# Optimization experiments

Measured on AMD Instinct MI355X. Metric: run time of the kernel, lower is better.

The kernel has to match this reference:

```python
import jax, jax.numpy as jnp
import numpy as np

HIDDEN = 1024
N_EMB = 4096
K_TOP = 64
EPS = 1e-6


def rmsnorm(x, w):
    xf = x.astype(jnp.float32)
    y = xf * jax.lax.rsqrt(jnp.mean(xf * xf, axis=-1, keepdims=True) + EPS)
    return y.astype(x.dtype) * w


def setup_inputs() -> dict:
    key = jax.random.key(0)
    ks = jax.random.split(key, 5)
    B, S, D, N = 16, 2048, HIDDEN, N_EMB
    bound = 1.0 / np.sqrt(D)  # torch Linear reset_parameters uniform bound
    return {
        "X": jax.random.normal(ks[0], (B, S, D), dtype=jnp.float32),
        "alpha": jnp.zeros((), dtype=jnp.float32),
        "E": jax.random.normal(ks[1], (N, D), dtype=jnp.float32) / np.sqrt(D),
        "Wq": jax.random.uniform(ks[2], (D, D), dtype=jnp.float32, minval=-bound, maxval=bound),
        "Wk": jax.random.uniform(ks[3], (D, D), dtype=jnp.float32, minval=-bound, maxval=bound),
        "xn_w": jnp.ones((D,), dtype=jnp.float32),
        "sn_w": jnp.ones((D,), dtype=jnp.float32),
        "on_w": jnp.ones((D,), dtype=jnp.float32),
    }


def reference(X, alpha, E, Wq, Wk, xn_w, sn_w, on_w):
    scale = HIDDEN ** (-0.5)
    Xn = rmsnorm(X, xn_w)            # (B,S,D)
    En = rmsnorm(E, sn_w)            # (N,D)
    Q = Xn @ Wq.T                    # (B,S,D)
    Km = En @ Wk.T                   # (N,D)
    scores = jnp.einsum('bsd,nd->bsn', Q, Km) * scale  # (B,S,N)
    global_scores = jnp.max(scores, axis=1)            # (B,N)
    top_vals, _ = jax.lax.top_k(global_scores, K_TOP)
    cutoff = top_vals[:, -1:]                          # (B,1)
    masked = jnp.where(global_scores >= cutoff, global_scores, -jnp.inf)
    dense_w = jax.nn.softmax(global_scores, axis=-1)
    sparse_w = jax.nn.softmax(masked, axis=-1)
    weights = alpha * dense_w + (1.0 - alpha) * sparse_w  # (B,N)
    O = rmsnorm(weights @ En, on_w)                      # (B,D)
    return O, weights
```

## Files before the change

### kernel.cpp

```cpp
#include <hip/hip_runtime.h>


namespace {

constexpr int D_DIM = 1024;
constexpr int NE    = 4096;
constexpr int BATCH = 16;
constexpr int SEQ   = 2048;
constexpr int MX    = BATCH * SEQ;
constexpr int KTOP  = 64;
constexpr int CAND  = 128;
constexpr int BK    = 32;

using f32x4  = __attribute__((ext_vector_type(4))) float;
using bf16x8 = __attribute__((ext_vector_type(8))) short;
using i32x4  = __attribute__((ext_vector_type(4))) int;

__device__ inline unsigned encf(float f) {
  unsigned u = __float_as_uint(f);
  return (u & 0x80000000u) ? ~u : (u | 0x80000000u);
}
__device__ inline float decf(unsigned e) {
  unsigned u = (e & 0x80000000u) ? (e ^ 0x80000000u) : ~e;
  return __uint_as_float(u);
}

__device__ inline unsigned short f2bf(float f) {
  unsigned u = __float_as_uint(f);
  unsigned lsb = (u >> 16) & 1u;
  u += 0x7fffu + lsb;
  return (unsigned short)(u >> 16);
}
__device__ inline float bf2f(unsigned short h) {
  return __uint_as_float(((unsigned)h) << 16);
}

__device__ inline void gload16(const void* gsrc, void* ldst) {
  __builtin_amdgcn_global_load_lds(
      (const __attribute__((address_space(1))) unsigned int*)gsrc,
      (__attribute__((address_space(3))) unsigned int*)ldst, 16, 0, 0);
}

#define LGK0_SB() do { asm volatile("s_waitcnt lgkmcnt(0)" ::: "memory"); \
                       __builtin_amdgcn_sched_barrier(0); } while (0)

__global__ void row_rinv_k(const float* __restrict__ X, float* __restrict__ rinv) {
  __shared__ float l4[4];
  int row = blockIdx.x;
  float4 v = ((const float4*)(X + (size_t)row * D_DIM))[threadIdx.x];
  float ss = v.x * v.x + v.y * v.y + v.z * v.z + v.w * v.w;
  for (int o = 32; o > 0; o >>= 1) ss += __shfl_xor(ss, o);
  int lane = threadIdx.x & 63, w = threadIdx.x >> 6;
  if (lane == 0) l4[w] = ss;
  __syncthreads();
  if (threadIdx.x == 0) {
    float t = l4[0] + l4[1] + l4[2] + l4[3];
    rinv[row] = rsqrtf(t * (1.0f / D_DIM) + 1e-6f);
  }
}

__global__ void rinv_quantx_k(const float* __restrict__ X, float* __restrict__ rinv,
                              float* __restrict__ sxr, int* __restrict__ XQ) {
  __shared__ float l4[4], m4[4];
  int row = blockIdx.x;
  float4 v = ((const float4*)(X + (size_t)row * D_DIM))[threadIdx.x];
  float ss = v.x * v.x + v.y * v.y + v.z * v.z + v.w * v.w;
  float am = fmaxf(fmaxf(fabsf(v.x), fabsf(v.y)), fmaxf(fabsf(v.z), fabsf(v.w)));
  for (int o = 32; o > 0; o >>= 1) {
    ss += __shfl_xor(ss, o);
    am = fmaxf(am, __shfl_xor(am, o));
  }
  int lane = threadIdx.x & 63, w = threadIdx.x >> 6;
  if (lane == 0) { l4[w] = ss; m4[w] = am; }
  __syncthreads();
  float t  = l4[0] + l4[1] + l4[2] + l4[3];
  float amax = fmaxf(fmaxf(m4[0], m4[1]), fmaxf(m4[2], m4[3]));
  amax = fmaxf(amax, 1e-30f);
  float ri = rsqrtf(t * (1.0f / D_DIM) + 1e-6f);
  if (threadIdx.x == 0) {
    rinv[row] = ri;
    sxr[row]  = ri * amax * (1.0f / 127.0f);
  }
  float qs = 127.0f / amax;
  int q0 = (int)rintf(v.x * qs) & 0xff;
  int q1 = (int)rintf(v.y * qs) & 0xff;
  int q2 = (int)rintf(v.z * qs) & 0xff;
  int q3 = (int)rintf(v.w * qs) & 0xff;
  XQ[(size_t)row * 256 + threadIdx.x] = q0 | (q1 << 8) | (q2 << 16) | (q3 << 24);
}

__global__ void quant_p_k(const unsigned short* __restrict__ PH,
                          const unsigned short* __restrict__ PL,
                          float* __restrict__ sp, int* __restrict__ PQ) {
  __shared__ float m4[4];
  int row = blockIdx.x;
  ushort4 h = *(const ushort4*)(PH + (size_t)row * D_DIM + threadIdx.x * 4);
  ushort4 l = *(const ushort4*)(PL + (size_t)row * D_DIM + threadIdx.x * 4);
  float p0 = bf2f(h.x) + bf2f(l.x);
  float p1 = bf2f(h.y) + bf2f(l.y);
  float p2 = bf2f(h.z) + bf2f(l.z);
  float p3 = bf2f(h.w) + bf2f(l.w);
  float am = fmaxf(fmaxf(fabsf(p0), fabsf(p1)), fmaxf(fabsf(p2), fabsf(p3)));
  for (int o = 32; o > 0; o >>= 1) am = fmaxf(am, __shfl_xor(am, o));
  int lane = threadIdx.x & 63, w = threadIdx.x >> 6;
  if (lane == 0) m4[w] = am;
  __syncthreads();
  float amax = fmaxf(fmaxf(m4[0], m4[1]), fmaxf(m4[2], m4[3]));
  amax = fmaxf(amax, 1e-30f);
  if (threadIdx.x == 0) sp[row] = amax * (1.0f / 127.0f);
  float qs = 127.0f / amax;
  int q0 = (int)rintf(p0 * qs) & 0xff;
  int q1 = (int)rintf(p1 * qs) & 0xff;
  int q2 = (int)rintf(p2 * qs) & 0xff;
  int q3 = (int)rintf(p3 * qs) & 0xff;
  PQ[(size_t)row * 256 + threadIdx.x] = q0 | (q1 << 8) | (q2 << 16) | (q3 << 24);
}

__global__ void split_wt_k(const float* __restrict__ W, const float* __restrict__ cw,
                           unsigned short* __restrict__ H, unsigned short* __restrict__ L) {
  __shared__ float t[32][33];
  int k0 = blockIdx.x * 32, d0 = blockIdx.y * 32;
  int tx = threadIdx.x & 31, ty4 = (threadIdx.x >> 5) * 4;
#pragma unroll
  for (int i = 0; i < 4; ++i)
    t[ty4 + i][tx] = W[(size_t)(d0 + ty4 + i) * D_DIM + k0 + tx];
  __syncthreads();
#pragma unroll
  for (int i = 0; i < 4; ++i) {
    int a = ty4 + i;
    float v = t[tx][a] * cw[k0 + a];
    unsigned short h = f2bf(v);
    H[(size_t)(k0 + a) * D_DIM + d0 + tx] = h;
    L[(size_t)(k0 + a) * D_DIM + d0 + tx] = f2bf(v - bf2f(h));
  }
}

__global__ void transpose_k(const float* __restrict__ W, float* __restrict__ T) {
  __shared__ float t[32][33];
  int x0 = blockIdx.x * 32, y0 = blockIdx.y * 32;
  int tx = threadIdx.x & 31, ty4 = (threadIdx.x >> 5) * 4;
#pragma unroll
  for (int i = 0; i < 4; ++i)
    t[ty4 + i][tx] = W[(size_t)(y0 + ty4 + i) * D_DIM + x0 + tx];
  __syncthreads();
#pragma unroll
  for (int i = 0; i < 4; ++i)
    T[(size_t)(x0 + ty4 + i) * D_DIM + y0 + tx] = t[tx][ty4 + i];
}

template <int FPOUT>
__global__ __launch_bounds__(256, 2) void gemm_a32_k(
    const float* __restrict__ A, const float* __restrict__ rinv,
    const unsigned short* __restrict__ BH, const unsigned short* __restrict__ BL,
    unsigned short* __restrict__ OH, unsigned short* __restrict__ OL,
    float* __restrict__ Of) {
  __shared__ __align__(16) float lA[128 * 32];
  __shared__ __align__(16) unsigned short lBH[128 * 32];
  __shared__ __align__(16) unsigned short lBL[128 * 32];
  __shared__ float ldsR[128];

  int tid = threadIdx.x;
  int lane = tid & 63, wid = tid >> 6;
  int wr = wid >> 1, wc = wid & 1;
  int fr = lane & 15, fg = lane >> 4;
  long m0 = (long)blockIdx.x * 128;
  long n0 = (long)blockIdx.y * 128;

  if (tid < 128) ldsR[tid] = rinv ? rinv[m0 + tid] : 1.0f;

  f32x4 acc[4][4] = {};

  for (int kk = 0; kk < D_DIM; kk += BK) {
#pragma unroll
    for (int i = 0; i < 4; ++i) {
      int chunk = i * 256 + tid;
      int r = chunk >> 3, c = chunk & 7;
      int cs = c ^ (r & 7);
      const float* src = A + (m0 + r) * (long)D_DIM + kk + cs * 4;
      gload16(src, (void*)(lA + ((i * 256 + (tid & ~63)) << 2)));
    }
#pragma unroll
    for (int i = 0; i < 2; ++i) {
      int chunk = i * 256 + tid;
      int r = chunk >> 2, c = chunk & 3;
      int cs = c ^ ((r >> 1) & 3);
      long boff = (n0 + r) * (long)D_DIM + kk + cs * 8;
      int lo = (i * 256 + (tid & ~63)) << 3;
      gload16(BH + boff, (void*)(lBH + lo));
      gload16(BL + boff, (void*)(lBL + lo));
    }
    __syncthreads();

    bf16x8 aH[4], aL[4], bH[4], bL[4];
#pragma unroll
    for (int m = 0; m < 4; ++m) {
      int row = wr * 64 + m * 16 + fr;
      int rm = row & 7;
      f32x4 p0 = *(const f32x4*)(lA + row * 32 + (((fg * 2 + 0) ^ rm) * 4));
      f32x4 p1 = *(const f32x4*)(lA + row * 32 + (((fg * 2 + 1) ^ rm) * 4));
#pragma unroll
      for (int e = 0; e < 8; ++e) {
        float f = (e < 4) ? p0[e] : p1[e - 4];
        unsigned short h = f2bf(f);
        aH[m][e] = (short)h;
        aL[m][e] = (short)f2bf(f - bf2f(h));
      }
    }
#pragma unroll
    for (int n = 0; n < 4; ++n) {
      int row = wc * 64 + n * 16 + fr;
      int sc = fg ^ ((row >> 1) & 3);
      bH[n] = *(const bf16x8*)(lBH + row * 32 + sc * 8);
      bL[n] = *(const bf16x8*)(lBL + row * 32 + sc * 8);
    }
#pragma unroll
    for (int m = 0; m < 4; ++m)
#pragma unroll
      for (int n = 0; n < 4; ++n) {
        acc[m][n] = __builtin_amdgcn_mfma_f32_16x16x32_bf16(aH[m], bH[n], acc[m][n], 0, 0, 0);
        acc[m][n] = __builtin_amdgcn_mfma_f32_16x16x32_bf16(aH[m], bL[n], acc[m][n], 0, 0, 0);
        acc[m][n] = __builtin_amdgcn_mfma_f32_16x16x32_bf16(aL[m], bH[n], acc[m][n], 0, 0, 0);
      }
    __syncthreads();
  }

#pragma unroll
  for (int m = 0; m < 4; ++m) {
#pragma unroll
    for (int j = 0; j < 4; ++j) {
      int rloc = wr * 64 + m * 16 + fg * 4 + j;
      float rv = ldsR[rloc];
      long grow = m0 + rloc;
#pragma unroll
      for (int n = 0; n < 4; ++n) {
        long gcol = n0 + wc * 64 + n * 16 + fr;
        float v = acc[m][n][j] * rv;
        if (FPOUT) {
          Of[grow * D_DIM + gcol] = v;
        } else {
          unsigned short h = f2bf(v);
          OH[grow * D_DIM + gcol] = h;
          OL[grow * D_DIM + gcol] = f2bf(v - bf2f(h));
        }
      }
    }
  }
}

__global__ __launch_bounds__(512, 2) void gemm_scores1_k(
    const signed char* __restrict__ XQ, const signed char* __restrict__ PQ,
    const float* __restrict__ sxr, const float* __restrict__ sp,
    unsigned* __restrict__ gmax) {
  __shared__ __align__(16) signed char lA[2][256 * 64];
  __shared__ __align__(16) signed char lB[2][256 * 64];
  __shared__ float ldsR[256];

  int tid = threadIdx.x;
  int lane = tid & 63, wid = tid >> 6;
  int wr = wid >> 2;
  int wcn = wid & 3;
  int fr = lane & 15, fg = lane >> 4;

  int id = blockIdx.x;
  int xcd = id & 7;
  int r = id >> 3;
  int tile_m = xcd * 16 + (r >> 4);
  int tile_n = r & 15;
  long m0 = (long)tile_m * 256;
  long n0 = (long)tile_n * 256;

  if (tid < 256) ldsR[tid] = sxr[m0 + tid];

  auto stageTile = [&](int buf, int kt) {
    int kk = kt * 64;
#pragma unroll
    for (int i = 0; i < 2; ++i) {
      int chunk = i * 512 + tid;
      int r2 = chunk >> 2, c = chunk & 3;
      int cs = c ^ ((r2 >> 1) & 3);
      gload16(XQ + (m0 + r2) * (long)D_DIM + kk + cs * 16,
              (void*)(&lA[buf][0] + ((i * 512 + (tid & ~63)) << 4)));
    }
#pragma unroll
    for (int i = 0; i < 2; ++i) {
      int chunk = i * 512 + tid;
      int r2 = chunk >> 2, c = chunk & 3;
      int cs = c ^ ((r2 >> 1) & 3);
      gload16(PQ + (n0 + r2) * (long)D_DIM + kk + cs * 16,
              (void*)(&lB[buf][0] + ((i * 512 + (tid & ~63)) << 4)));
    }
  };

  i32x4 acc[8][4] = {};

  stageTile(0, 0);
  stageTile(1, 1);
  asm volatile("s_waitcnt lgkmcnt(0)" ::: "memory");

  i32x4 aF[4], bF[4];

  for (int kt = 0; kt < 16; ++kt) {
    int cur = kt & 1;
    const signed char* As = &lA[cur][0];
    const signed char* Bs = &lB[cur][0];

    if (kt < 15) {
      asm volatile("s_waitcnt vmcnt(4)" ::: "memory");
    } else {
      asm volatile("s_waitcnt vmcnt(0)" ::: "memory");
    }
    __builtin_amdgcn_s_barrier();

#pragma unroll
    for (int mi = 0; mi < 4; ++mi) {
      int row = wr * 128 + mi * 16 + fr;
      int ck = fg ^ ((row >> 1) & 3);
      aF[mi] = *(const i32x4*)(As + row * 64 + ck * 16);
    }
#pragma unroll
    for (int ni = 0; ni < 2; ++ni) {
      int row = wcn * 64 + ni * 16 + fr;
      int ck = fg ^ ((row >> 1) & 3);
      bF[ni] = *(const i32x4*)(Bs + row * 64 + ck * 16);
    }
    LGK0_SB();
    __builtin_amdgcn_s_setprio(1);
#pragma unroll
    for (int mi = 0; mi < 4; ++mi)
#pragma unroll
      for (int ni = 0; ni < 2; ++ni)
        acc[mi][ni] = __builtin_amdgcn_mfma_i32_16x16x64_i8(
            aF[mi], bF[ni], acc[mi][ni], 0, 0, 0);
    __builtin_amdgcn_s_setprio(0);

#pragma unroll
    for (int ni = 2; ni < 4; ++ni) {
      int row = wcn * 64 + ni * 16 + fr;
      int ck = fg ^ ((row >> 1) & 3);
      bF[ni] = *(const i32x4*)(Bs + row * 64 + ck * 16);
    }
    LGK0_SB();
    __builtin_amdgcn_s_setprio(1);
#pragma unroll
    for (int mi = 0; mi < 4; ++mi)
#pragma unroll
      for (int ni = 2; ni < 4; ++ni)
        acc[mi][ni] = __builtin_amdgcn_mfma_i32_16x16x64_i8(
            aF[mi], bF[ni], acc[mi][ni], 0, 0, 0);
    __builtin_amdgcn_s_setprio(0);

#pragma unroll
    for (int mi = 0; mi < 4; ++mi) {
      int row = wr * 128 + (mi + 4) * 16 + fr;
      int ck = fg ^ ((row >> 1) & 3);
      aF[mi] = *(const i32x4*)(As + row * 64 + ck * 16);
    }
    LGK0_SB();
    __builtin_amdgcn_s_barrier();
    if (kt + 2 < 16) stageTile(cur, kt + 2);
    __builtin_amdgcn_s_setprio(1);
#pragma unroll
    for (int mi = 0; mi < 4; ++mi)
#pragma unroll
      for (int ni = 2; ni < 4; ++ni)
        acc[mi + 4][ni] = __builtin_amdgcn_mfma_i32_16x16x64_i8(
            aF[mi], bF[ni], acc[mi + 4][ni], 0, 0, 0);
    __builtin_amdgcn_s_setprio(0);

    __builtin_amdgcn_s_setprio(1);
#pragma unroll
    for (int mi = 0; mi < 4; ++mi)
#pragma unroll
      for (int ni = 0; ni < 2; ++ni)
        acc[mi + 4][ni] = __builtin_amdgcn_mfma_i32_16x16x64_i8(
            aF[mi], bF[ni], acc[mi + 4][ni], 0, 0, 0);
    __builtin_amdgcn_s_setprio(0);
  }

  int b = (int)(m0 >> 11);
#pragma unroll
  for (int ni = 0; ni < 4; ++ni) {
    long col = n0 + wcn * 64 + ni * 16 + fr;
    float spc = sp[col];
    float v = -3.0e38f;
#pragma unroll
    for (int mi = 0; mi < 8; ++mi)
#pragma unroll
      for (int j = 0; j < 4; ++j) {
        int row = wr * 128 + mi * 16 + fg * 4 + j;
        v = fmaxf(v, (float)acc[mi][ni][j] * ldsR[row]);
      }
    v *= spc;
    v = fmaxf(v, __shfl_xor(v, 16));
    v = fmaxf(v, __shfl_xor(v, 32));
    if (fg == 0) {
      atomicMax(&gmax[(long)b * NE + col], encf(v * 0.03125f));
    }
  }
}

__global__ void cand_select_k(const unsigned* __restrict__ gmax,
                              int* __restrict__ candIdx, unsigned* __restrict__ gmax2) {
  __shared__ unsigned enc[NE];
  __shared__ int ic[257];
  int tid = threadIdx.x;
  int lane = tid & 63, w = tid >> 6;
  int zb = blockIdx.x;
  if (tid < CAND) gmax2[zb * CAND + tid] = 0u;
  const unsigned* g = gmax + (size_t)zb * NE;
  for (int i = tid; i < NE; i += 256) enc[i] = g[i];
  __syncthreads();

  unsigned cur = 0;
  for (int bit = 31; bit >= 0; --bit) {
    unsigned cand = cur | (1u << bit);
    int c = 0;
    for (int i = tid; i < NE; i += 256) c += (enc[i] >= cand) ? 1 : 0;
    for (int o = 32; o > 0; o >>= 1) c += __shfl_xor(c, o);
    __syncthreads();
    if (lane == 0) ic[w] = c;
    __syncthreads();
    int tot = ic[0] + ic[1] + ic[2] + ic[3];
    if (tot >= CAND) cur = cand;
  }

  int myc = 0;
  for (int i = tid; i < NE; i += 256) myc += (enc[i] >= cur) ? 1 : 0;
  __syncthreads();
  ic[tid] = myc;
  __syncthreads();
  if (tid == 0) {
    int s = 0;
    for (int t = 0; t < 256; ++t) { int v = ic[t]; ic[t] = s; s += v; }
  }
  __syncthreads();
  int off = ic[tid];
  for (int i = tid; i < NE; i += 256)
    if (enc[i] >= cur) {
      if (off < CAND) candIdx[zb * CAND + off] = i;
      ++off;
    }
}

__global__ void gather_k(const unsigned short* __restrict__ PH,
                         const unsigned short* __restrict__ PL,
                         const int* __restrict__ candIdx,
                         unsigned short* __restrict__ cPH,
                         unsigned short* __restrict__ cPL) {
  int j = blockIdx.x;
  int zb = blockIdx.y;
  int n = candIdx[zb * CAND + j];
  int t4 = threadIdx.x * 4;
  size_t dst = ((size_t)(zb * CAND + j)) * D_DIM + t4;
  size_t src = (size_t)n * D_DIM + t4;
  *(ushort4*)(cPH + dst) = *(const ushort4*)(PH + src);
  *(ushort4*)(cPL + dst) = *(const ushort4*)(PL + src);
}

__global__ __launch_bounds__(256, 2) void gemm_rescore_k(
    const float* __restrict__ X, const float* __restrict__ rinvA,
    const unsigned short* __restrict__ cPH, const unsigned short* __restrict__ cPL,
    unsigned* __restrict__ gmax2) {
  __shared__ __align__(16) float lA[128 * 32];
  __shared__ __align__(16) unsigned short lBH[128 * 32], lBL[128 * 32];
  __shared__ float ldsR[128];

  int tid = threadIdx.x;
  int lane = tid & 63, wid = tid >> 6;
  int wr = wid >> 1, wc = wid & 1;
  int fr = lane & 15, fg = lane >> 4;
  int z = blockIdx.z;
  long m0 = (long)blockIdx.x * 128;
  long arow0 = (long)z * SEQ + m0;
  long brow0 = (long)z * CAND;

  if (tid < 128) ldsR[tid] = rinvA[arow0 + tid];

  f32x4 acc[4][4] = {};

  for (int kk = 0; kk < D_DIM; kk += BK) {
#pragma unroll
    for (int i = 0; i < 4; ++i) {
      int chunk = i * 256 + tid;
      int r = chunk >> 3, c = chunk & 7;
      int cs = c ^ (r & 7);
      const float* src = X + (arow0 + r) * (long)D_DIM + kk + cs * 4;
      gload16(src, (void*)(lA + ((i * 256 + (tid & ~63)) << 2)));
    }
#pragma unroll
    for (int i = 0; i < 2; ++i) {
      int chunk = i * 256 + tid;
      int r = chunk >> 2, c = chunk & 3;
      int cs = c ^ ((r >> 1) & 3);
      long boff = (brow0 + r) * (long)D_DIM + kk + cs * 8;
      int lo = (i * 256 + (tid & ~63)) << 3;
      gload16(cPH + boff, (void*)(lBH + lo));
      gload16(cPL + boff, (void*)(lBL + lo));
    }
    __syncthreads();

    bf16x8 aH[4], aL[4], bH[4], bL[4];
#pragma unroll
    for (int m = 0; m < 4; ++m) {
      int row = wr * 64 + m * 16 + fr;
      int rm = row & 7;
      f32x4 p0 = *(const f32x4*)(lA + row * 32 + (((fg * 2 + 0) ^ rm) * 4));
      f32x4 p1 = *(const f32x4*)(lA + row * 32 + (((fg * 2 + 1) ^ rm) * 4));
#pragma unroll
      for (int e = 0; e < 8; ++e) {
        float f = (e < 4) ? p0[e] : p1[e - 4];
        unsigned short h = f2bf(f);
        aH[m][e] = (short)h;
        aL[m][e] = (short)f2bf(f - bf2f(h));
      }
    }
#pragma unroll
    for (int n = 0; n < 4; ++n) {
      int row = wc * 64 + n * 16 + fr;
      int sc = fg ^ ((row >> 1) & 3);
      bH[n] = *(const bf16x8*)(lBH + row * 32 + sc * 8);
      bL[n] = *(const bf16x8*)(lBL + row * 32 + sc * 8);
    }
#pragma unroll
    for (int m = 0; m < 4; ++m)
#pragma unroll
      for (int n = 0; n < 4; ++n) {
        acc[m][n] = __builtin_amdgcn_mfma_f32_16x16x32_bf16(aH[m], bH[n], acc[m][n], 0, 0, 0);
        acc[m][n] = __builtin_amdgcn_mfma_f32_16x16x32_bf16(aH[m], bL[n], acc[m][n], 0, 0, 0);
        acc[m][n] = __builtin_amdgcn_mfma_f32_16x16x32_bf16(aL[m], bH[n], acc[m][n], 0, 0, 0);
      }
    __syncthreads();
  }

#pragma unroll
  for (int n = 0; n < 4; ++n) {
    float v = -3.0e38f;
#pragma unroll
    for (int m = 0; m < 4; ++m)
#pragma unroll
      for (int j = 0; j < 4; ++j) {
        float rv = ldsR[wr * 64 + m * 16 + fg * 4 + j];
        v = fmaxf(v, acc[m][n][j] * rv);
      }
    v = fmaxf(v, __shfl_xor(v, 16));
    v = fmaxf(v, __shfl_xor(v, 32));
    if (fg == 0) {
      int col = wc * 64 + n * 16 + fr;
      atomicMax(&gmax2[z * CAND + col], encf(v * 0.03125f));
    }
  }
}

__global__ void scatter_k(const unsigned* __restrict__ gmax2,
                          const int* __restrict__ candIdx,
                          unsigned* __restrict__ gmax) {
  int z = blockIdx.x, j = threadIdx.x;
  int n = candIdx[z * CAND + j];
  gmax[(size_t)z * NE + n] = gmax2[z * CAND + j];
}

__global__ void topk_weights_k(const unsigned* __restrict__ gmax,
                               const float* __restrict__ alpha_p,
                               float* __restrict__ wout, int* __restrict__ idx,
                               int* __restrict__ cnt) {
  __shared__ unsigned enc[NE];
  __shared__ unsigned ubc[4];
  __shared__ float l4[4];
  __shared__ int ic[257];
  int tid = threadIdx.x;
  int lane = tid & 63, w = tid >> 6;
  const unsigned* g = gmax + (size_t)blockIdx.x * NE;
  for (int i = tid; i < NE; i += 256) enc[i] = g[i];
  __syncthreads();

  unsigned mx = 0;
  for (int i = tid; i < NE; i += 256) mx = enc[i] > mx ? enc[i] : mx;
  for (int o = 32; o > 0; o >>= 1) {
    unsigned other = (unsigned)__shfl_xor((int)mx, o);
    if (other > mx) mx = other;
  }
  if (lane == 0) ubc[w] = mx;
  __syncthreads();
  unsigned m1e = ubc[0];
  for (int t = 1; t < 4; ++t) m1e = ubc[t] > m1e ? ubc[t] : m1e;
  float m1 = decf(m1e);

  unsigned cur = 0;
  for (int bit = 31; bit >= 0; --bit) {
    unsigned cand = cur | (1u << bit);
    int c = 0;
    for (int i = tid; i < NE; i += 256) c += (enc[i] >= cand) ? 1 : 0;
    for (int o = 32; o > 0; o >>= 1) c += __shfl_xor(c, o);
    __syncthreads();
    if (lane == 0) ic[w] = c;
    __syncthreads();
    int tot = ic[0] + ic[1] + ic[2] + ic[3];
    if (tot >= KTOP) cur = cand;
  }

  float sd = 0.f, ssum = 0.f;
  for (int i = tid; i < NE; i += 256) {
    float e = expf(decf(enc[i]) - m1);
    sd += e;
    if (enc[i] >= cur) ssum += e;
  }
  for (int o = 32; o > 0; o >>= 1) { sd += __shfl_xor(sd, o); ssum += __shfl_xor(ssum, o); }
  __syncthreads();
  if (lane == 0) { l4[w] = sd; }
  __syncthreads();
  float SD = l4[0] + l4[1] + l4[2] + l4[3];
  __syncthreads();
  if (lane == 0) { l4[w] = ssum; }
  __syncthreads();
  float SS = l4[0] + l4[1] + l4[2] + l4[3];

  float alpha = alpha_p[0];
  float wd = alpha / SD;
  float ws_ = (1.0f - alpha) / SS;
  for (int i = tid; i < NE; i += 256) {
    float e = expf(decf(enc[i]) - m1);
    float wv = wd * e + ((enc[i] >= cur) ? ws_ * e : 0.0f);
    wout[(size_t)blockIdx.x * NE + i] = wv;
  }

  int myc = 0;
  for (int i = tid; i < NE; i += 256) myc += (enc[i] >= cur) ? 1 : 0;
  __syncthreads();
  ic[tid] = myc;
  __syncthreads();
  if (tid == 0) {
    int s = 0;
    for (int t = 0; t < 256; ++t) { int v = ic[t]; ic[t] = s; s += v; }
    ic[256] = s;
    cnt[blockIdx.x] = s;
  }
  __syncthreads();
  int off = ic[tid];
  for (int i = tid; i < NE; i += 256)
    if (enc[i] >= cur) idx[(size_t)blockIdx.x * NE + (off++)] = i;
}

__global__ void out_o_k(const float* __restrict__ wts, const float* __restrict__ E,
                        const float* __restrict__ rinvE, const float* __restrict__ sn_w,
                        const float* __restrict__ on_w, const float* __restrict__ alpha_p,
                        const int* __restrict__ idx, const int* __restrict__ cnt,
                        float* __restrict__ O) {
  __shared__ float l4[4];
  int b = blockIdx.x, tid = threadIdx.x;
  float acc[4] = {0.f, 0.f, 0.f, 0.f};
  float alpha = alpha_p[0];
  if (alpha == 0.0f) {
    int nsel = cnt[b];
    for (int j = 0; j < nsel; ++j) {
      int n = idx[(size_t)b * NE + j];
      float wv = wts[(size_t)b * NE + n] * rinvE[n];
      const float* er = E + (size_t)n * D_DIM;
#pragma unroll
      for (int i = 0; i < 4; ++i) acc[i] += wv * er[tid + 256 * i];
    }
  } else {
    for (int n = 0; n < NE; ++n) {
      float wv = wts[(size_t)b * NE + n] * rinvE[n];
      const float* er = E + (size_t)n * D_DIM;
#pragma unroll
      for (int i = 0; i < 4; ++i) acc[i] += wv * er[tid + 256 * i];
    }
  }
  float ssq = 0.f;
#pragma unroll
  for (int i = 0; i < 4; ++i) {
    acc[i] *= sn_w[tid + 256 * i];
    ssq += acc[i] * acc[i];
  }
  for (int o = 32; o > 0; o >>= 1) ssq += __shfl_xor(ssq, o);
  int lane = tid & 63, w = tid >> 6;
  if (lane == 0) l4[w] = ssq;
  __syncthreads();
  float tot = l4[0] + l4[1] + l4[2] + l4[3];
  float r = rsqrtf(tot * (1.0f / D_DIM) + 1e-6f);
#pragma unroll
  for (int i = 0; i < 4; ++i)
    O[(size_t)b * D_DIM + tid + 256 * i] = acc[i] * r * on_w[tid + 256 * i];
}

}

extern "C" void kernel_launch(void* const* d_in, const int* in_sizes, int n_in,
                              void* d_out, int out_size, void* d_ws, size_t ws_size,
                              hipStream_t stream) {
  const float* X     = (const float*)d_in[0];
  const float* alpha = (const float*)d_in[1];
  const float* E     = (const float*)d_in[2];
  const float* Wq    = (const float*)d_in[3];
  const float* Wk    = (const float*)d_in[4];
  const float* xn_w  = (const float*)d_in[5];
  const float* sn_w  = (const float*)d_in[6];
  const float* on_w  = (const float*)d_in[7];
  float* O    = (float*)d_out;
  float* Wout = (float*)d_out + (size_t)BATCH * D_DIM;

  char* ws = (char*)d_ws;
  size_t off = 0;
  auto alloc = [&](size_t bytes) {
    char* p = ws + off;
    off += (bytes + 255) & ~(size_t)255;
    return p;
  };
  signed char*    XQ    = (signed char*)alloc((size_t)MX * D_DIM);
  signed char*    PQ    = (signed char*)alloc((size_t)NE * D_DIM);
  float*          WqTf  = (float*)alloc((size_t)D_DIM * D_DIM * 4);
  unsigned short* WkTH  = (unsigned short*)alloc((size_t)D_DIM * D_DIM * 2);
  unsigned short* WkTL  = (unsigned short*)alloc((size_t)D_DIM * D_DIM * 2);
  unsigned short* W2TH  = (unsigned short*)alloc((size_t)D_DIM * D_DIM * 2);
  unsigned short* W2TL  = (unsigned short*)alloc((size_t)D_DIM * D_DIM * 2);
  unsigned short* PH    = (unsigned short*)alloc((size_t)NE * D_DIM * 2);
  unsigned short* PL    = (unsigned short*)alloc((size_t)NE * D_DIM * 2);
  unsigned short* cPH   = (unsigned short*)alloc((size_t)BATCH * CAND * D_DIM * 2);
  unsigned short* cPL   = (unsigned short*)alloc((size_t)BATCH * CAND * D_DIM * 2);
  float* rinvX = (float*)alloc((size_t)MX * 4);
  float* sxr   = (float*)alloc((size_t)MX * 4);
  float* rinvE = (float*)alloc((size_t)NE * 4);
  float* sp    = (float*)alloc((size_t)NE * 4);
  unsigned* gmax  = (unsigned*)alloc((size_t)BATCH * NE * 4);
  unsigned* gmax2 = (unsigned*)alloc((size_t)BATCH * CAND * 4);
  int* candIdx = (int*)alloc((size_t)BATCH * CAND * 4);
  int* idx = (int*)alloc((size_t)BATCH * NE * 4);
  int* cnt = (int*)alloc((size_t)BATCH * 4);
  if (off > ws_size) return;

  hipMemsetAsync(gmax, 0, (size_t)BATCH * NE * 4, stream);

  row_rinv_k<<<NE, 256, 0, stream>>>(E, rinvE);
  transpose_k<<<dim3(D_DIM / 32, D_DIM / 32), 256, 0, stream>>>(Wq, WqTf);
  split_wt_k<<<dim3(D_DIM / 32, D_DIM / 32), 256, 0, stream>>>(Wk, sn_w, WkTH, WkTL);
  gemm_a32_k<0><<<dim3(8, 8), 256, 0, stream>>>(
      WqTf, xn_w, WkTH, WkTL, W2TH, W2TL, nullptr);
  gemm_a32_k<0><<<dim3(NE / 128, D_DIM / 128), 256, 0, stream>>>(
      E, rinvE, W2TH, W2TL, PH, PL, nullptr);
  quant_p_k<<<NE, 256, 0, stream>>>(PH, PL, sp, (int*)PQ);

  rinv_quantx_k<<<MX, 256, 0, stream>>>(X, rinvX, sxr, (int*)XQ);
  gemm_scores1_k<<<(MX / 256) * (NE / 256), 512, 0, stream>>>(XQ, PQ, sxr, sp, gmax);

  cand_select_k<<<BATCH, 256, 0, stream>>>(gmax, candIdx, gmax2);
  gather_k<<<dim3(CAND, BATCH), 256, 0, stream>>>(PH, PL, candIdx, cPH, cPL);
  gemm_rescore_k<<<dim3(SEQ / 128, 1, BATCH), 256, 0, stream>>>(
      X, rinvX, cPH, cPL, gmax2);
  scatter_k<<<BATCH, CAND, 0, stream>>>(gmax2, candIdx, gmax);

  topk_weights_k<<<BATCH, 256, 0, stream>>>(gmax, alpha, Wout, idx, cnt);
  out_o_k<<<BATCH, 256, 0, stream>>>(Wout, E, rinvE, sn_w, on_w, alpha, idx, cnt, O);
}
```

Measured before the change: 438.3 us.

## Fuse small kernels, gather candidate rows in-GEMM, and reorder score tile schedule

Merges the Wq transpose and Wk split into one prep kernel, and drops the separate gather kernel so the rescore GEMM reads candidate rows of PH/PL directly through candIdx. It merges scatter, top-k weights and output accumulation into one final kernel that keeps the selection in shared memory. It also changes the block-to-tile mapping in the int8 scores GEMM to alter cache locality. Together these cut launch count and intermediate global traffic, at the cost of more shared memory in the final kernel and non-contiguous B loads in the rescore GEMM.

New measurement: 415.9 us. -5.1%, faster.

```diff
diff --git a/kernel.cpp b/kernel.cpp
--- a/kernel.cpp
+++ b/kernel.cpp
@@ -116,36 +116,27 @@
   PQ[(size_t)row * 256 + threadIdx.x] = q0 | (q1 << 8) | (q2 << 16) | (q3 << 24);
 }
 
-__global__ void split_wt_k(const float* __restrict__ W, const float* __restrict__ cw,
-                           unsigned short* __restrict__ H, unsigned short* __restrict__ L) {
-  __shared__ float t[32][33];
+__global__ void prep_w_k(const float* __restrict__ Wq, const float* __restrict__ Wk,
+                         const float* __restrict__ cw, float* __restrict__ T,
+                         unsigned short* __restrict__ H, unsigned short* __restrict__ L) {
+  __shared__ float t[32][33], u[32][33];
   int k0 = blockIdx.x * 32, d0 = blockIdx.y * 32;
   int tx = threadIdx.x & 31, ty4 = (threadIdx.x >> 5) * 4;
 #pragma unroll
-  for (int i = 0; i < 4; ++i)
-    t[ty4 + i][tx] = W[(size_t)(d0 + ty4 + i) * D_DIM + k0 + tx];
+  for (int i = 0; i < 4; ++i) {
+    t[ty4 + i][tx] = Wq[(size_t)(d0 + ty4 + i) * D_DIM + k0 + tx];
+    u[ty4 + i][tx] = Wk[(size_t)(d0 + ty4 + i) * D_DIM + k0 + tx];
+  }
   __syncthreads();
 #pragma unroll
   for (int i = 0; i < 4; ++i) {
     int a = ty4 + i;
-    float v = t[tx][a] * cw[k0 + a];
+    T[(size_t)(k0 + a) * D_DIM + d0 + tx] = t[tx][a];
+    float v = u[tx][a] * cw[k0 + a];
     unsigned short h = f2bf(v);
     H[(size_t)(k0 + a) * D_DIM + d0 + tx] = h;
     L[(size_t)(k0 + a) * D_DIM + d0 + tx] = f2bf(v - bf2f(h));
   }
-}
-
-__global__ void transpose_k(const float* __restrict__ W, float* __restrict__ T) {
-  __shared__ float t[32][33];
-  int x0 = blockIdx.x * 32, y0 = blockIdx.y * 32;
-  int tx = threadIdx.x & 31, ty4 = (threadIdx.x >> 5) * 4;
-#pragma unroll
-  for (int i = 0; i < 4; ++i)
-    t[ty4 + i][tx] = W[(size_t)(y0 + ty4 + i) * D_DIM + x0 + tx];
-  __syncthreads();
-#pragma unroll
-  for (int i = 0; i < 4; ++i)
-    T[(size_t)(x0 + ty4 + i) * D_DIM + y0 + tx] = t[tx][ty4 + i];
 }
 
 template <int FPOUT>
@@ -264,8 +255,8 @@
   int id = blockIdx.x;
   int xcd = id & 7;
   int r = id >> 3;
-  int tile_m = xcd * 16 + (r >> 4);
-  int tile_n = r & 15;
+  int tile_n = (r & 7) | ((r >> 7) << 3);
+  int tile_m = xcd * 16 + ((r >> 3) & 15);
   long m0 = (long)tile_m * 256;
   long n0 = (long)tile_n * 256;
 
@@ -442,25 +433,10 @@
     }
 }
 
-__global__ void gather_k(const unsigned short* __restrict__ PH,
-                         const unsigned short* __restrict__ PL,
-                         const int* __restrict__ candIdx,
-                         unsigned short* __restrict__ cPH,
-                         unsigned short* __restrict__ cPL) {
-  int j = blockIdx.x;
-  int zb = blockIdx.y;
-  int n = candIdx[zb * CAND + j];
-  int t4 = threadIdx.x * 4;
-  size_t dst = ((size_t)(zb * CAND + j)) * D_DIM + t4;
-  size_t src = (size_t)n * D_DIM + t4;
-  *(ushort4*)(cPH + dst) = *(const ushort4*)(PH + src);
-  *(ushort4*)(cPL + dst) = *(const ushort4*)(PL + src);
-}
-
 __global__ __launch_bounds__(256, 2) void gemm_rescore_k(
     const float* __restrict__ X, const float* __restrict__ rinvA,
-    const unsigned short* __restrict__ cPH, const unsigned short* __restrict__ cPL,
-    unsigned* __restrict__ gmax2) {
+    const unsigned short* __restrict__ PH, const unsigned short* __restrict__ PL,
+    const int* __restrict__ candIdx, unsigned* __restrict__ gmax2) {
   __shared__ __align__(16) float lA[128 * 32];
   __shared__ __align__(16) unsigned short lBH[128 * 32], lBL[128 * 32];
   __shared__ float ldsR[128];
@@ -472,9 +448,15 @@
   int z = blockIdx.z;
   long m0 = (long)blockIdx.x * 128;
   long arow0 = (long)z * SEQ + m0;
-  long brow0 = (long)z * CAND;
 
   if (tid < 128) ldsR[tid] = rinvA[arow0 + tid];
+
+  long bbase[2];
+#pragma unroll
+  for (int i = 0; i < 2; ++i) {
+    int r = (i * 256 + tid) >> 2;
+    bbase[i] = (long)candIdx[z * CAND + r] * D_DIM;
+  }
 
   f32x4 acc[4][4] = {};
 
@@ -492,10 +474,10 @@
       int chunk = i * 256 + tid;
       int r = chunk >> 2, c = chunk & 3;
       int cs = c ^ ((r >> 1) & 3);
-      long boff = (brow0 + r) * (long)D_DIM + kk + cs * 8;
+      long boff = bbase[i] + kk + cs * 8;
       int lo = (i * 256 + (tid & ~63)) << 3;
-      gload16(cPH + boff, (void*)(lBH + lo));
-      gload16(cPL + boff, (void*)(lBL + lo));
+      gload16(PH + boff, (void*)(lBH + lo));
+      gload16(PL + boff, (void*)(lBL + lo));
     }
     __syncthreads();
 
@@ -551,26 +533,25 @@
   }
 }
 
-__global__ void scatter_k(const unsigned* __restrict__ gmax2,
-                          const int* __restrict__ candIdx,
-                          unsigned* __restrict__ gmax) {
-  int z = blockIdx.x, j = threadIdx.x;
-  int n = candIdx[z * CAND + j];
-  gmax[(size_t)z * NE + n] = gmax2[z * CAND + j];
-}
-
-__global__ void topk_weights_k(const unsigned* __restrict__ gmax,
-                               const float* __restrict__ alpha_p,
-                               float* __restrict__ wout, int* __restrict__ idx,
-                               int* __restrict__ cnt) {
+__global__ void final_k(const unsigned* __restrict__ gmax,
+                        const unsigned* __restrict__ gmax2,
+                        const int* __restrict__ candIdx,
+                        const float* __restrict__ alpha_p,
+                        const float* __restrict__ E, const float* __restrict__ rinvE,
+                        const float* __restrict__ sn_w, const float* __restrict__ on_w,
+                        float* __restrict__ wout, float* __restrict__ O) {
   __shared__ unsigned enc[NE];
+  __shared__ int sel[NE];
   __shared__ unsigned ubc[4];
   __shared__ float l4[4];
   __shared__ int ic[257];
   int tid = threadIdx.x;
   int lane = tid & 63, w = tid >> 6;
-  const unsigned* g = gmax + (size_t)blockIdx.x * NE;
+  int b = blockIdx.x;
+  const unsigned* g = gmax + (size_t)b * NE;
   for (int i = tid; i < NE; i += 256) enc[i] = g[i];
+  __syncthreads();
+  if (tid < CAND) enc[candIdx[b * CAND + tid]] = gmax2[b * CAND + tid];
   __syncthreads();
 
   unsigned mx = 0;
@@ -620,7 +601,7 @@
   for (int i = tid; i < NE; i += 256) {
     float e = expf(decf(enc[i]) - m1);
     float wv = wd * e + ((enc[i] >= cur) ? ws_ * e : 0.0f);
-    wout[(size_t)blockIdx.x * NE + i] = wv;
+    wout[(size_t)b * NE + i] = wv;
   }
 
   int myc = 0;
@@ -632,35 +613,29 @@
     int s = 0;
     for (int t = 0; t < 256; ++t) { int v = ic[t]; ic[t] = s; s += v; }
     ic[256] = s;
-    cnt[blockIdx.x] = s;
   }
   __syncthreads();
   int off = ic[tid];
   for (int i = tid; i < NE; i += 256)
-    if (enc[i] >= cur) idx[(size_t)blockIdx.x * NE + (off++)] = i;
-}
-
-__global__ void out_o_k(const float* __restrict__ wts, const float* __restrict__ E,
-                        const float* __restrict__ rinvE, const float* __restrict__ sn_w,
-                        const float* __restrict__ on_w, const float* __restrict__ alpha_p,
-                        const int* __restrict__ idx, const int* __restrict__ cnt,
-                        float* __restrict__ O) {
-  __shared__ float l4[4];
-  int b = blockIdx.x, tid = threadIdx.x;
+    if (enc[i] >= cur) sel[off++] = i;
+  __syncthreads();
+  int nsel = ic[256];
+
   float acc[4] = {0.f, 0.f, 0.f, 0.f};
-  float alpha = alpha_p[0];
   if (alpha == 0.0f) {
-    int nsel = cnt[b];
+    float coef = wd + ws_;
     for (int j = 0; j < nsel; ++j) {
-      int n = idx[(size_t)b * NE + j];
-      float wv = wts[(size_t)b * NE + n] * rinvE[n];
+      int n = sel[j];
+      float e = expf(decf(enc[n]) - m1);
+      float wv = coef * e * rinvE[n];
       const float* er = E + (size_t)n * D_DIM;
 #pragma unroll
       for (int i = 0; i < 4; ++i) acc[i] += wv * er[tid + 256 * i];
     }
   } else {
     for (int n = 0; n < NE; ++n) {
-      float wv = wts[(size_t)b * NE + n] * rinvE[n];
+      float e = expf(decf(enc[n]) - m1);
+      float wv = (wd * e + ((enc[n] >= cur) ? ws_ * e : 0.0f)) * rinvE[n];
       const float* er = E + (size_t)n * D_DIM;
 #pragma unroll
       for (int i = 0; i < 4; ++i) acc[i] += wv * er[tid + 256 * i];
@@ -673,14 +648,13 @@
     ssq += acc[i] * acc[i];
   }
   for (int o = 32; o > 0; o >>= 1) ssq += __shfl_xor(ssq, o);
-  int lane = tid & 63, w = tid >> 6;
   if (lane == 0) l4[w] = ssq;
   __syncthreads();
   float tot = l4[0] + l4[1] + l4[2] + l4[3];
-  float r = rsqrtf(tot * (1.0f / D_DIM) + 1e-6f);
+  float rn = rsqrtf(tot * (1.0f / D_DIM) + 1e-6f);
 #pragma unroll
   for (int i = 0; i < 4; ++i)
-    O[(size_t)b * D_DIM + tid + 256 * i] = acc[i] * r * on_w[tid + 256 * i];
+    O[(size_t)b * D_DIM + tid + 256 * i] = acc[i] * rn * on_w[tid + 256 * i];
 }
 
 }
@@ -715,8 +689,6 @@
   unsigned short* W2TL  = (unsigned short*)alloc((size_t)D_DIM * D_DIM * 2);
   unsigned short* PH    = (unsigned short*)alloc((size_t)NE * D_DIM * 2);
   unsigned short* PL    = (unsigned short*)alloc((size_t)NE * D_DIM * 2);
-  unsigned short* cPH   = (unsigned short*)alloc((size_t)BATCH * CAND * D_DIM * 2);
-  unsigned short* cPL   = (unsigned short*)alloc((size_t)BATCH * CAND * D_DIM * 2);
   float* rinvX = (float*)alloc((size_t)MX * 4);
   float* sxr   = (float*)alloc((size_t)MX * 4);
   float* rinvE = (float*)alloc((size_t)NE * 4);
@@ -724,15 +696,13 @@
   unsigned* gmax  = (unsigned*)alloc((size_t)BATCH * NE * 4);
   unsigned* gmax2 = (unsigned*)alloc((size_t)BATCH * CAND * 4);
   int* candIdx = (int*)alloc((size_t)BATCH * CAND * 4);
-  int* idx = (int*)alloc((size_t)BATCH * NE * 4);
-  int* cnt = (int*)alloc((size_t)BATCH * 4);
   if (off > ws_size) return;
 
   hipMemsetAsync(gmax, 0, (size_t)BATCH * NE * 4, stream);
 
   row_rinv_k<<<NE, 256, 0, stream>>>(E, rinvE);
-  transpose_k<<<dim3(D_DIM / 32, D_DIM / 32), 256, 0, stream>>>(Wq, WqTf);
-  split_wt_k<<<dim3(D_DIM / 32, D_DIM / 32), 256, 0, stream>>>(Wk, sn_w, WkTH, WkTL);
+  prep_w_k<<<dim3(D_DIM / 32, D_DIM / 32), 256, 0, stream>>>(
+      Wq, Wk, sn_w, WqTf, WkTH, WkTL);
   gemm_a32_k<0><<<dim3(8, 8), 256, 0, stream>>>(
       WqTf, xn_w, WkTH, WkTL, W2TH, W2TL, nullptr);
   gemm_a32_k<0><<<dim3(NE / 128, D_DIM / 128), 256, 0, stream>>>(
@@ -743,11 +713,8 @@
   gemm_scores1_k<<<(MX / 256) * (NE / 256), 512, 0, stream>>>(XQ, PQ, sxr, sp, gmax);
 
   cand_select_k<<<BATCH, 256, 0, stream>>>(gmax, candIdx, gmax2);
-  gather_k<<<dim3(CAND, BATCH), 256, 0, stream>>>(PH, PL, candIdx, cPH, cPL);
   gemm_rescore_k<<<dim3(SEQ / 128, 1, BATCH), 256, 0, stream>>>(
-      X, rinvX, cPH, cPL, gmax2);
-  scatter_k<<<BATCH, CAND, 0, stream>>>(gmax2, candIdx, gmax);
-
-  topk_weights_k<<<BATCH, 256, 0, stream>>>(gmax, alpha, Wout, idx, cnt);
-  out_o_k<<<BATCH, 256, 0, stream>>>(Wout, E, rinvE, sn_w, on_w, alpha, idx, cnt, O);
-}
+      X, rinvX, PH, PL, candIdx, gmax2);
+  final_k<<<BATCH, 256, 0, stream>>>(gmax, gmax2, candIdx, alpha, E, rinvE,
+                                     sn_w, on_w, Wout, O);
+}
```
